# Optimization experiments

Measured on AMD Instinct MI355X. Metric: run time of the kernel, lower is better.

## Reference

```python
import jax, jax.numpy as jnp
import numpy as np

B, S, H = 16, 2048, 1024

def setup_inputs() -> dict:
    key = jax.random.key(0)
    ks = jax.random.split(key, 6)
    return {
        "h": jax.random.normal(ks[0], (1, B, H), jnp.float32),
        "c": jax.random.normal(ks[1], (1, B, H), jnp.float32),
        "encoder_outputs": jax.random.normal(ks[2], (B, S, H), jnp.float32),
        "attn_W": jax.random.normal(ks[3], (H, 2 * H), jnp.float32) * 0.02,
        "attn_b": jax.random.normal(ks[4], (H,), jnp.float32) * 0.02,
        "v_W": jax.random.normal(ks[5], (1, H), jnp.float32) * 0.02,
    }

def reference(h, c, encoder_outputs, attn_W, attn_b, v_W):
    # h: (1,B,H) -> (B,1,H); a: (B,S,H)
    a = encoder_outputs
    hq = jnp.transpose(h, (1, 0, 2))  # (B,1,H)
    # cat((s, a), -1) @ attn_W.T == s @ Wh.T + a @ Wa.T (avoids (B,S,2H) buffer)
    Wh, Wa = attn_W[:, :H], attn_W[:, H:]
    energy = jax.nn.relu(
        jnp.einsum("bqh,oh->bqo", hq, Wh)          # (B,1,H), broadcast over S
        + jnp.einsum("bsh,oh->bso", a, Wa)
        + attn_b
    )  # (B,S,H)
    scores = jnp.einsum("bsh,h->bs", energy, v_W[0])  # (B,S)
    attn_weights = jax.nn.softmax(scores, axis=1)      # (B,S)
    context = jnp.einsum("bs,bsh->bh", attn_weights, a)[:, None, :]  # (B,1,H)
    return context, attn_weights
```

## Files before the change

kernel.cpp:

```cpp
#include <hip/hip_runtime.h>
#include <hip/hip_bf16.h>


typedef __bf16 bf16x8 __attribute__((ext_vector_type(8)));
typedef float floatx4 __attribute__((ext_vector_type(4)));

#define BB 16
#define SS 2048
#define HH 1024
#define MM (BB * SS)

#define GLB(p) ((const __attribute__((address_space(1))) void*)(p))
#define LDSP(p) ((__attribute__((address_space(3))) void*)(p))

__device__ inline ushort f2bf(float x) {
    uint32_t u = __builtin_bit_cast(uint32_t, x);
    u += 0x7FFFu + ((u >> 16) & 1u);
    return (ushort)(u >> 16);
}

__global__ __launch_bounds__(256) void prep_all_kernel(
    const float* __restrict__ h, const float* __restrict__ W,
    const float* __restrict__ bias, const float* __restrict__ a,
    float* __restrict__ projh, __bf16* __restrict__ Wb, __bf16* __restrict__ Ab,
    float* __restrict__ sp0, float* __restrict__ ctx)
{
    int bid = blockIdx.x;
    int tid = threadIdx.x;
    if (bid >= 336) {
        size_t i = (size_t)(bid - 336) * 256 + tid;
        const float* s = a + i * 8;
        float4 x = *(const float4*)(s);
        float4 y = *(const float4*)(s + 4);
        union { ushort u[8]; uint4 v; } p;
        p.u[0] = f2bf(x.x); p.u[1] = f2bf(x.y); p.u[2] = f2bf(x.z); p.u[3] = f2bf(x.w);
        p.u[4] = f2bf(y.x); p.u[5] = f2bf(y.y); p.u[6] = f2bf(y.z); p.u[7] = f2bf(y.w);
        *(uint4*)(Ab + i * 8) = p.v;
    } else if (bid < 256) {
        int b = bid >> 4;
        int oc = bid & 15;
        __shared__ float hrow[HH];
        *(float4*)&hrow[tid * 4] = *(const float4*)(h + (size_t)b * HH + tid * 4);
        __syncthreads();
        int ol = tid >> 2;
        int kq = tid & 3;
        int o = oc * 64 + ol;
        const float* wr = W + (size_t)o * (2 * HH) + kq * 256;
        const float* hb = hrow + kq * 256;
        float sum = 0.f;
        for (int k = 0; k < 256; k += 4) {
            float4 wv = *(const float4*)(wr + k);
            sum += hb[k] * wv.x + hb[k + 1] * wv.y + hb[k + 2] * wv.z + hb[k + 3] * wv.w;
        }
        sum += __shfl_xor(sum, 1);
        sum += __shfl_xor(sum, 2);
        if (kq == 0) projh[b * HH + o] = sum + bias[o];
    } else if (bid < 320) {
        int cb = bid - 256;
#pragma unroll
        for (int j = 0; j < 8; j++) {
            int g = cb * 2048 + tid + j * 256;
            int o = g >> 7;
            int k = (g & 127) * 8;
            const float* s = W + (size_t)o * (2 * HH) + HH + k;
            float4 x = *(const float4*)(s);
            float4 y = *(const float4*)(s + 4);
            union { ushort u[8]; uint4 v; } p;
            p.u[0] = f2bf(x.x); p.u[1] = f2bf(x.y); p.u[2] = f2bf(x.z); p.u[3] = f2bf(x.w);
            p.u[4] = f2bf(y.x); p.u[5] = f2bf(y.y); p.u[6] = f2bf(y.z); p.u[7] = f2bf(y.w);
            *(uint4*)(Wb + (size_t)o * HH + k) = p.v;
        }
    } else {
        int zb = bid - 320;
        float4 z = make_float4(0.f, 0.f, 0.f, 0.f);
        float* sp = sp0 + zb * 2048 + tid * 8;
        *(float4*)(sp) = z;
        *(float4*)(sp + 4) = z;
        *(float4*)(ctx + zb * 1024 + tid * 4) = z;
    }
}

__global__ __launch_bounds__(512, 2) void gemm_scores_kernel(
    const __bf16* __restrict__ Ab,
    const __bf16* __restrict__ Wb,
    const float* __restrict__ projh,
    const float* __restrict__ vW,
    float* __restrict__ scores_part)
{
    __shared__ __bf16 smem[65536];

    const int bid = blockIdx.x;
    const int m0 = (((bid >> 5) << 3) + (bid & 7)) * 256;
    const int nq = (bid >> 3) & 3;
    const int n0 = nq * 256;
    const int bidx = m0 >> 11;

    const int tid = threadIdx.x;
    const int lane = tid & 63;
    const int wave = tid >> 6;
    const int wm = (wave & 1) * 128;
    const int wn = (wave >> 1) * 64;
    const int quad = lane >> 4;
    const int l16 = lane & 15;

    floatx4 acc[8][4];
    const floatx4 z = {0.f, 0.f, 0.f, 0.f};
#pragma unroll
    for (int i = 0; i < 8; i++)
#pragma unroll
        for (int j = 0; j < 4; j++) acc[i][j] = z;

    const int su = tid >> 3;
    const int sj = (tid & 7) ^ (su & 7);
    const int g_row = su * 2 + (sj >> 2);
    const int g_col = (sj & 3) * 8;
    const __bf16* gA0 = Ab + (size_t)(m0 + g_row) * HH + g_col;
    const __bf16* gA1 = gA0 + (size_t)128 * HH;
    const __bf16* gB0 = Wb + (size_t)(n0 + g_row) * HH + g_col;
    const __bf16* gB1 = gB0 + (size_t)128 * HH;
    const int wchunk = wave * 512;

    int aoff[8], boff[4];
#pragma unroll
    for (int i = 0; i < 8; i++) {
        int frow = wm + i * 16 + l16;
        int r7 = frow & 127;
        int u2 = r7 >> 1;
        int cc = u2 * 8 + (((((r7 & 1) << 2) | quad)) ^ (u2 & 7));
        aoff[i] = (frow >> 7) * 4096 + cc * 8;
    }
#pragma unroll
    for (int j = 0; j < 4; j++) {
        int frow = wn + j * 16 + l16;
        int r7 = frow & 127;
        int u2 = r7 >> 1;
        int cc = u2 * 8 + (((((r7 & 1) << 2) | quad)) ^ (u2 & 7));
        boff[j] = 32768 + (frow >> 7) * 4096 + cc * 8;
    }

#define STAGE_A(slot, koff)                                                             \
    {                                                                                   \
        __bf16* d_ = smem + (slot) * 8192 + wchunk;                                     \
        __builtin_amdgcn_global_load_lds(GLB(gA0 + (koff)), LDSP(d_), 16, 0, 0);        \
        __builtin_amdgcn_global_load_lds(GLB(gA1 + (koff)), LDSP(d_ + 4096), 16, 0, 0); \
    }
#define STAGE_B(slot, koff)                                                             \
    {                                                                                   \
        __bf16* d_ = smem + 32768 + (slot) * 8192 + wchunk;                             \
        __builtin_amdgcn_global_load_lds(GLB(gB0 + (koff)), LDSP(d_), 16, 0, 0);        \
        __builtin_amdgcn_global_load_lds(GLB(gB1 + (koff)), LDSP(d_ + 4096), 16, 0, 0); \
    }
#define READ_BFR(base)                                     \
    {                                                      \
        bfr[0] = *(const bf16x8*)((base) + boff[0]);       \
        bfr[1] = *(const bf16x8*)((base) + boff[1]);       \
        bfr[2] = *(const bf16x8*)((base) + boff[2]);       \
        bfr[3] = *(const bf16x8*)((base) + boff[3]);       \
    }
#define READ_ALO(base)                                     \
    {                                                      \
        af[0] = *(const bf16x8*)((base) + aoff[0]);        \
        af[1] = *(const bf16x8*)((base) + aoff[1]);        \
        af[2] = *(const bf16x8*)((base) + aoff[2]);        \
        af[3] = *(const bf16x8*)((base) + aoff[3]);        \
    }
#define READ_AHI(base)                                     \
    {                                                      \
        af2[0] = *(const bf16x8*)((base) + aoff[4]);       \
        af2[1] = *(const bf16x8*)((base) + aoff[5]);       \
        af2[2] = *(const bf16x8*)((base) + aoff[6]);       \
        af2[3] = *(const bf16x8*)((base) + aoff[7]);       \
    }
#define MFMA_LO                                                                            \
    _Pragma("unroll") for (int i_ = 0; i_ < 4; i_++)                                       \
        _Pragma("unroll") for (int j_ = 0; j_ < 4; j_++)                                   \
            acc[i_][j_] = __builtin_amdgcn_mfma_f32_16x16x32_bf16(af[i_], bfr[j_], acc[i_][j_], 0, 0, 0);
#define MFMA_HI                                                                            \
    _Pragma("unroll") for (int i_ = 0; i_ < 4; i_++)                                       \
        _Pragma("unroll") for (int j_ = 0; j_ < 4; j_++)                                   \
            acc[i_ + 4][j_] = __builtin_amdgcn_mfma_f32_16x16x32_bf16(af2[i_], bfr[j_], acc[i_ + 4][j_], 0, 0, 0);
#define BAR __builtin_amdgcn_s_barrier()
#define LGKM0 asm volatile("s_waitcnt lgkmcnt(0)" ::: "memory")
#define VM8 asm volatile("s_waitcnt vmcnt(8)" ::: "memory")
#define PRIO1 __builtin_amdgcn_s_setprio(1)
#define PRIO0 __builtin_amdgcn_s_setprio(0)

#define SPAN(P, K1, K2)                              \
    {                                                \
        const __bf16* cb0 = smem + (P) * 16384;      \
        const __bf16* cb1 = cb0 + 8192;              \
                                        \
        READ_BFR(cb0); READ_ALO(cb0);                \
        STAGE_A((1 - (P)) * 2 + 1, K1);              \
        BAR; LGKM0; PRIO1; MFMA_LO; PRIO0; BAR;      \
                                        \
        READ_AHI(cb0);                               \
        STAGE_B((1 - (P)) * 2 + 1, K1);              \
        VM8;                                         \
        BAR; LGKM0; PRIO1; MFMA_HI; PRIO0; BAR;      \
                                        \
        READ_BFR(cb1); READ_ALO(cb1);                \
        STAGE_A((P) * 2, K2);                        \
        BAR; LGKM0; PRIO1; MFMA_LO; PRIO0; BAR;      \
                                        \
        READ_AHI(cb1);                               \
        STAGE_B((P) * 2, K2);                        \
        VM8;                                         \
        BAR; LGKM0; PRIO1; MFMA_HI; PRIO0; BAR;      \
    }

    bf16x8 af[4], af2[4], bfr[4];

    STAGE_A(0, 0);  STAGE_B(0, 0);
    STAGE_A(1, 32); STAGE_B(1, 32);
    STAGE_A(2, 64); STAGE_B(2, 64);
    VM8;
    BAR;

    for (int it = 0; it < 8; ++it) {
        const int kb = it * 128;
        const int k1 = kb + 96;
        const int k2 = (it < 7) ? kb + 128 : 0;
        const int k3 = (it < 7) ? kb + 160 : 0;
        const int k4 = (it < 7) ? kb + 192 : 0;
        SPAN(0, k1, k2)
        SPAN(1, k3, k4)
    }

#undef SPAN
#undef STAGE_A
#undef STAGE_B
#undef READ_BFR
#undef READ_ALO
#undef READ_AHI
#undef MFMA_LO
#undef MFMA_HI
#undef BAR
#undef LGKM0
#undef VM8
#undef PRIO1
#undef PRIO0

    float ph[4], vv[4];
#pragma unroll
    for (int j = 0; j < 4; j++) {
        int ng = n0 + wn + j * 16 + l16;
        ph[j] = projh[bidx * HH + ng];
        vv[j] = vW[ng];
    }

    float* red = (float*)smem;
    if (tid < 256) red[tid] = 0.f;
    __syncthreads();

#pragma unroll
    for (int i = 0; i < 8; i++) {
        float s[4] = {0.f, 0.f, 0.f, 0.f};
#pragma unroll
        for (int j = 0; j < 4; j++) {
#pragma unroll
            for (int r2 = 0; r2 < 4; r2++) {
                float e = acc[i][j][r2] + ph[j];
                e = e > 0.f ? e : 0.f;
                s[r2] += e * vv[j];
            }
        }
#pragma unroll
        for (int r2 = 0; r2 < 4; r2++) {
            s[r2] += __shfl_xor(s[r2], 1);
            s[r2] += __shfl_xor(s[r2], 2);
            s[r2] += __shfl_xor(s[r2], 4);
            s[r2] += __shfl_xor(s[r2], 8);
        }
        if (l16 == 0) {
#pragma unroll
            for (int r2 = 0; r2 < 4; r2++)
                atomicAdd(&red[wm + i * 16 + quad * 4 + r2], s[r2]);
        }
    }
    __syncthreads();
    if (tid < 256) scores_part[(size_t)nq * MM + m0 + tid] = red[tid];
}

__global__ __launch_bounds__(256) void gemm_scores_f32_kernel(
    const float* __restrict__ A, const float* __restrict__ W,
    const float* __restrict__ projh, const float* __restrict__ vW,
    float* __restrict__ scores)
{
    constexpr int BM = 128, BN = 128, BK = 32, LDT = BK + 8;
    __shared__ __bf16 As[BM * LDT];
    __shared__ __bf16 Bs[BN * LDT];
    const int n0 = blockIdx.x * BN;
    const int m0 = blockIdx.y * BM;
    const int bidx = m0 >> 11;
    const int tid = threadIdx.x;
    const int lane = tid & 63;
    const int wave = tid >> 6;
    const int wm = (wave & 1) * 64;
    const int wn = (wave >> 1) * 64;
    const int quad = lane >> 4;
    const int l16 = lane & 15;
    floatx4 acc[4][4];
    const floatx4 z = {0.f, 0.f, 0.f, 0.f};
#pragma unroll
    for (int i = 0; i < 4; i++)
#pragma unroll
        for (int j = 0; j < 4; j++) acc[i][j] = z;
    int rowT[4], colT[4];
#pragma unroll
    for (int i = 0; i < 4; i++) {
        int fi = tid + 256 * i;
        rowT[i] = fi >> 3;
        colT[i] = (fi & 7) * 4;
    }
    for (int k0 = 0; k0 < HH; k0 += BK) {
        float4 av[4], bv[4];
#pragma unroll
        for (int i = 0; i < 4; i++) {
            av[i] = *(const float4*)(A + (size_t)(m0 + rowT[i]) * HH + k0 + colT[i]);
            bv[i] = *(const float4*)(W + (size_t)(n0 + rowT[i]) * (2 * HH) + HH + k0 + colT[i]);
        }
        __syncthreads();
#pragma unroll
        for (int i = 0; i < 4; i++) {
            ushort4 ua = make_ushort4(f2bf(av[i].x), f2bf(av[i].y), f2bf(av[i].z), f2bf(av[i].w));
            ushort4 ub = make_ushort4(f2bf(bv[i].x), f2bf(bv[i].y), f2bf(bv[i].z), f2bf(bv[i].w));
            *(ushort4*)&As[rowT[i] * LDT + colT[i]] = ua;
            *(ushort4*)&Bs[rowT[i] * LDT + colT[i]] = ub;
        }
        __syncthreads();
        bf16x8 af[4], bf[4];
#pragma unroll
        for (int i = 0; i < 4; i++)
            af[i] = *(const bf16x8*)&As[(wm + i * 16 + l16) * LDT + quad * 8];
#pragma unroll
        for (int j = 0; j < 4; j++)
            bf[j] = *(const bf16x8*)&Bs[(wn + j * 16 + l16) * LDT + quad * 8];
#pragma unroll
        for (int i = 0; i < 4; i++)
#pragma unroll
            for (int j = 0; j < 4; j++)
                acc[i][j] = __builtin_amdgcn_mfma_f32_16x16x32_bf16(af[i], bf[j], acc[i][j], 0, 0, 0);
    }
    float ph[4], vv[4];
#pragma unroll
    for (int j = 0; j < 4; j++) {
        int ng = n0 + wn + j * 16 + l16;
        ph[j] = projh[bidx * HH + ng];
        vv[j] = vW[ng];
    }
#pragma unroll
    for (int i = 0; i < 4; i++) {
        float s[4] = {0.f, 0.f, 0.f, 0.f};
#pragma unroll
        for (int j = 0; j < 4; j++) {
#pragma unroll
            for (int r = 0; r < 4; r++) {
                float e = acc[i][j][r] + ph[j];
                e = e > 0.f ? e : 0.f;
                s[r] += e * vv[j];
            }
        }
#pragma unroll
        for (int r = 0; r < 4; r++) {
            s[r] += __shfl_xor(s[r], 1);
            s[r] += __shfl_xor(s[r], 2);
            s[r] += __shfl_xor(s[r], 4);
            s[r] += __shfl_xor(s[r], 8);
        }
        if (l16 == 0) {
#pragma unroll
            for (int r = 0; r < 4; r++) {
                int mg = m0 + wm + i * 16 + quad * 4 + r;
                atomicAdd(&scores[mg], s[r]);
            }
        }
    }
}

__global__ __launch_bounds__(256) void softmax_context_kernel(
    const __bf16* __restrict__ Ab, const float* __restrict__ scores_part,
    int nparts, float* __restrict__ wout, float* __restrict__ ctx)
{
    int b = blockIdx.x >> 5;
    int sc = blockIdx.x & 31;
    int tid = threadIdx.x;
    const float* srow = scores_part + b * SS;

    float x[8];
    float mx = -1e30f;
#pragma unroll
    for (int i = 0; i < 8; i++) {
        int idx = tid + i * 256;
        float v = srow[idx];
        for (int q = 1; q < nparts; q++) v += srow[(size_t)q * MM + idx];
        x[i] = v; mx = fmaxf(mx, v);
    }
#pragma unroll
    for (int off = 32; off; off >>= 1) mx = fmaxf(mx, __shfl_xor(mx, off));
    __shared__ float redm[4], reds[4];
    if ((tid & 63) == 0) redm[tid >> 6] = mx;
    __syncthreads();
    mx = fmaxf(fmaxf(redm[0], redm[1]), fmaxf(redm[2], redm[3]));
    float sum = 0.f;
#pragma unroll
    for (int i = 0; i < 8; i++) sum += __expf(x[i] - mx);
#pragma unroll
    for (int off = 32; off; off >>= 1) sum += __shfl_xor(sum, off);
    if ((tid & 63) == 0) reds[tid >> 6] = sum;
    __syncthreads();
    float inv = 1.0f / (reds[0] + reds[1] + reds[2] + reds[3]);

    __shared__ float wsm[64];
    if (tid < 64) {
        int idx = sc * 64 + tid;
        float v = srow[idx];
        for (int q = 1; q < nparts; q++) v += srow[(size_t)q * MM + idx];
        float wv = __expf(v - mx) * inv;
        wsm[tid] = wv;
        wout[b * SS + idx] = wv;
    }
    __syncthreads();

    const __bf16* arow = Ab + ((size_t)b * SS + sc * 64) * HH + tid * 4;
    float4 acc = make_float4(0.f, 0.f, 0.f, 0.f);
#pragma unroll 4
    for (int s = 0; s < 64; s++) {
        float w = wsm[s];
        uint2 uv = *(const uint2*)(arow + (size_t)s * HH);
        float a0 = __builtin_bit_cast(float, uv.x << 16);
        float a1 = __builtin_bit_cast(float, uv.x & 0xffff0000u);
        float a2 = __builtin_bit_cast(float, uv.y << 16);
        float a3 = __builtin_bit_cast(float, uv.y & 0xffff0000u);
        acc.x += w * a0; acc.y += w * a1; acc.z += w * a2; acc.w += w * a3;
    }
    float* o = ctx + b * HH + tid * 4;
    atomicAdd(o + 0, acc.x);
    atomicAdd(o + 1, acc.y);
    atomicAdd(o + 2, acc.z);
    atomicAdd(o + 3, acc.w);
}

__global__ __launch_bounds__(256) void softmax_context_f32_kernel(
    const float* __restrict__ A, const float* __restrict__ scores_part,
    float* __restrict__ wout, float* __restrict__ ctx)
{
    int b = blockIdx.x >> 5;
    int sc = blockIdx.x & 31;
    int tid = threadIdx.x;
    const float* srow = scores_part + b * SS;
    float x[8];
    float mx = -1e30f;
#pragma unroll
    for (int i = 0; i < 8; i++) { x[i] = srow[tid + i * 256]; mx = fmaxf(mx, x[i]); }
#pragma unroll
    for (int off = 32; off; off >>= 1) mx = fmaxf(mx, __shfl_xor(mx, off));
    __shared__ float redm[4], reds[4];
    if ((tid & 63) == 0) redm[tid >> 6] = mx;
    __syncthreads();
    mx = fmaxf(fmaxf(redm[0], redm[1]), fmaxf(redm[2], redm[3]));
    float sum = 0.f;
#pragma unroll
    for (int i = 0; i < 8; i++) sum += __expf(x[i] - mx);
#pragma unroll
    for (int off = 32; off; off >>= 1) sum += __shfl_xor(sum, off);
    if ((tid & 63) == 0) reds[tid >> 6] = sum;
    __syncthreads();
    float inv = 1.0f / (reds[0] + reds[1] + reds[2] + reds[3]);
    __shared__ float wsm[64];
    if (tid < 64) {
        float wv = __expf(srow[sc * 64 + tid] - mx) * inv;
        wsm[tid] = wv;
        wout[b * SS + sc * 64 + tid] = wv;
    }
    __syncthreads();
    const float* arow = A + ((size_t)b * SS + sc * 64) * HH + tid * 4;
    float4 acc = make_float4(0.f, 0.f, 0.f, 0.f);
#pragma unroll 4
    for (int s = 0; s < 64; s++) {
        float w = wsm[s];
        float4 v = *(const float4*)(arow + (size_t)s * HH);
        acc.x += w * v.x; acc.y += w * v.y; acc.z += w * v.z; acc.w += w * v.w;
    }
    float* o = ctx + b * HH + tid * 4;
    atomicAdd(o + 0, acc.x);
    atomicAdd(o + 1, acc.y);
    atomicAdd(o + 2, acc.z);
    atomicAdd(o + 3, acc.w);
}

extern "C" void kernel_launch(void* const* d_in, const int* in_sizes, int n_in,
                              void* d_out, int out_size, void* d_ws, size_t ws_size,
                              hipStream_t stream) {
    const float* h    = (const float*)d_in[0];
    const float* a    = (const float*)d_in[2];
    const float* W    = (const float*)d_in[3];
    const float* bias = (const float*)d_in[4];
    const float* vW   = (const float*)d_in[5];
    float* out = (float*)d_out;

    float* projh       = (float*)d_ws;
    float* scores_part = projh + BB * HH;
    __bf16* Wb = (__bf16*)(scores_part + 4 * MM);
    __bf16* Ab = Wb + (size_t)HH * HH;
    const size_t need = (size_t)(BB * HH + 4 * MM) * 4 + (size_t)HH * HH * 2
                      + (size_t)MM * HH * 2;

    if (ws_size >= need) {
        prep_all_kernel<<<336 + MM * HH / 8 / 256, 256, 0, stream>>>(
            h, W, bias, a, projh, Wb, Ab, scores_part, out);
        gemm_scores_kernel<<<512, 512, 0, stream>>>(Ab, Wb, projh, vW, scores_part);
        softmax_context_kernel<<<BB * 32, 256, 0, stream>>>(
            Ab, scores_part, 4, out + BB * HH, out);
    } else {
        prep_all_kernel<<<336, 256, 0, stream>>>(h, W, bias, a, projh, Wb, Ab, scores_part, out);
        gemm_scores_f32_kernel<<<dim3(HH / 128, MM / 128), 256, 0, stream>>>(
            a, W, projh, vW, scores_part);
        softmax_context_f32_kernel<<<BB * 32, 256, 0, stream>>>(
            a, scores_part, out + BB * HH, out);
    }
}
```

Baseline: 292.3 us.

## Fuse fp32-to-bf16 conversion of encoder outputs into GEMM A-tile staging

Removes the separate prep pass that converted the full encoder_outputs tensor to bf16. The GEMM now loads fp32 A tiles into registers, converts them and writes them to LDS. Blocks with nq==0 also write the bf16 copy to global memory for the later softmax/context kernel. This saves one full fp32 read and bf16 write pass over the 128MB input. In exchange, A loads go through registers instead of direct global-to-LDS copies, with new vmcnt waits, and each A tile is read in fp32 by all four N-quarter blocks.

After: 319.2 us. 1.09x slower.

```diff
diff --git a/kernel.cpp b/kernel.cpp
--- a/kernel.cpp
+++ b/kernel.cpp
@@ -21,22 +21,13 @@
 
 __global__ __launch_bounds__(256) void prep_all_kernel(
     const float* __restrict__ h, const float* __restrict__ W,
-    const float* __restrict__ bias, const float* __restrict__ a,
-    float* __restrict__ projh, __bf16* __restrict__ Wb, __bf16* __restrict__ Ab,
+    const float* __restrict__ bias,
+    float* __restrict__ projh, __bf16* __restrict__ Wb,
     float* __restrict__ sp0, float* __restrict__ ctx)
 {
     int bid = blockIdx.x;
     int tid = threadIdx.x;
-    if (bid >= 336) {
-        size_t i = (size_t)(bid - 336) * 256 + tid;
-        const float* s = a + i * 8;
-        float4 x = *(const float4*)(s);
-        float4 y = *(const float4*)(s + 4);
-        union { ushort u[8]; uint4 v; } p;
-        p.u[0] = f2bf(x.x); p.u[1] = f2bf(x.y); p.u[2] = f2bf(x.z); p.u[3] = f2bf(x.w);
-        p.u[4] = f2bf(y.x); p.u[5] = f2bf(y.y); p.u[6] = f2bf(y.z); p.u[7] = f2bf(y.w);
-        *(uint4*)(Ab + i * 8) = p.v;
-    } else if (bid < 256) {
+    if (bid < 256) {
         int b = bid >> 4;
         int oc = bid & 15;
         __shared__ float hrow[HH];
@@ -81,11 +72,12 @@
 }
 
 __global__ __launch_bounds__(512, 2) void gemm_scores_kernel(
-    const __bf16* __restrict__ Ab,
+    const float* __restrict__ Af,
     const __bf16* __restrict__ Wb,
     const float* __restrict__ projh,
     const float* __restrict__ vW,
-    float* __restrict__ scores_part)
+    float* __restrict__ scores_part,
+    __bf16* __restrict__ Ab)
 {
     __shared__ __bf16 smem[65536];
 
@@ -114,8 +106,10 @@
     const int sj = (tid & 7) ^ (su & 7);
     const int g_row = su * 2 + (sj >> 2);
     const int g_col = (sj & 3) * 8;
-    const __bf16* gA0 = Ab + (size_t)(m0 + g_row) * HH + g_col;
-    const __bf16* gA1 = gA0 + (size_t)128 * HH;
+    const float* gAf0 = Af + (size_t)(m0 + g_row) * HH + g_col;
+    const float* gAf1 = gAf0 + (size_t)128 * HH;
+    __bf16* abw0 = Ab + (size_t)(m0 + g_row) * HH + g_col;
+    __bf16* abw1 = abw0 + (size_t)128 * HH;
     const __bf16* gB0 = Wb + (size_t)(n0 + g_row) * HH + g_col;
     const __bf16* gB1 = gB0 + (size_t)128 * HH;
     const int wchunk = wave * 512;
@@ -138,17 +132,36 @@
         boff[j] = 32768 + (frow >> 7) * 4096 + cc * 8;
     }
 
-#define STAGE_A(slot, koff)                                                             \
-    {                                                                                   \
-        __bf16* d_ = smem + (slot) * 8192 + wchunk;                                     \
-        __builtin_amdgcn_global_load_lds(GLB(gA0 + (koff)), LDSP(d_), 16, 0, 0);        \
-        __builtin_amdgcn_global_load_lds(GLB(gA1 + (koff)), LDSP(d_ + 4096), 16, 0, 0); \
-    }
-#define STAGE_B(slot, koff)                                                             \
+#define BGLOAD(slot, koff)                                                              \
     {                                                                                   \
         __bf16* d_ = smem + 32768 + (slot) * 8192 + wchunk;                             \
         __builtin_amdgcn_global_load_lds(GLB(gB0 + (koff)), LDSP(d_), 16, 0, 0);        \
         __builtin_amdgcn_global_load_lds(GLB(gB1 + (koff)), LDSP(d_ + 4096), 16, 0, 0); \
+    }
+#define AISSUE(K)                                      \
+    {                                                  \
+        ar0 = *(const float4*)(gAf0 + (K));            \
+        ar1 = *(const float4*)(gAf0 + (K) + 4);        \
+        ar2 = *(const float4*)(gAf1 + (K));            \
+        ar3 = *(const float4*)(gAf1 + (K) + 4);        \
+    }
+#define AWRITE(x0, x1, x2, x3, slot, K, WBOK)                                           \
+    {                                                                                   \
+        union { ushort u[8]; uint4 v; } pl_, ph_;                                       \
+        pl_.u[0] = f2bf((x0).x); pl_.u[1] = f2bf((x0).y);                               \
+        pl_.u[2] = f2bf((x0).z); pl_.u[3] = f2bf((x0).w);                               \
+        pl_.u[4] = f2bf((x1).x); pl_.u[5] = f2bf((x1).y);                               \
+        pl_.u[6] = f2bf((x1).z); pl_.u[7] = f2bf((x1).w);                               \
+        ph_.u[0] = f2bf((x2).x); ph_.u[1] = f2bf((x2).y);                               \
+        ph_.u[2] = f2bf((x2).z); ph_.u[3] = f2bf((x2).w);                               \
+        ph_.u[4] = f2bf((x3).x); ph_.u[5] = f2bf((x3).y);                               \
+        ph_.u[6] = f2bf((x3).z); ph_.u[7] = f2bf((x3).w);                               \
+        *(uint4*)(smem + (slot) * 8192 + tid * 8) = pl_.v;                              \
+        *(uint4*)(smem + (slot) * 8192 + 4096 + tid * 8) = ph_.v;                       \
+        if ((WBOK) && nq == 0) {                                                        \
+            *(uint4*)(abw0 + (K)) = pl_.v;                                              \
+            *(uint4*)(abw1 + (K)) = ph_.v;                                              \
+        }                                                                               \
     }
 #define READ_BFR(base)                                     \
     {                                                      \
@@ -181,55 +194,80 @@
             acc[i_ + 4][j_] = __builtin_amdgcn_mfma_f32_16x16x32_bf16(af2[i_], bfr[j_], acc[i_ + 4][j_], 0, 0, 0);
 #define BAR __builtin_amdgcn_s_barrier()
 #define LGKM0 asm volatile("s_waitcnt lgkmcnt(0)" ::: "memory")
-#define VM8 asm volatile("s_waitcnt vmcnt(8)" ::: "memory")
+#define VMW2 asm volatile("s_waitcnt vmcnt(2)" ::: "memory")
+#define VMW8 asm volatile("s_waitcnt vmcnt(8)" ::: "memory")
+#define VMW0 asm volatile("s_waitcnt vmcnt(0)" ::: "memory")
 #define PRIO1 __builtin_amdgcn_s_setprio(1)
 #define PRIO0 __builtin_amdgcn_s_setprio(0)
 
-#define SPAN(P, K1, K2)                              \
+#define SPAN(P, K1, K2, K3, WB1, WB2)                \
     {                                                \
         const __bf16* cb0 = smem + (P) * 16384;      \
         const __bf16* cb1 = cb0 + 8192;              \
                                         \
         READ_BFR(cb0); READ_ALO(cb0);                \
-        STAGE_A((1 - (P)) * 2 + 1, K1);              \
+        VMW2;                                        \
+        AWRITE(ar0, ar1, ar2, ar3, (1 - (P)) * 2 + 1, K1, WB1); \
+        AISSUE(K2);                                  \
         BAR; LGKM0; PRIO1; MFMA_LO; PRIO0; BAR;      \
                                         \
         READ_AHI(cb0);                               \
-        STAGE_B((1 - (P)) * 2 + 1, K1);              \
-        VM8;                                         \
+        BGLOAD((1 - (P)) * 2 + 1, K1);               \
         BAR; LGKM0; PRIO1; MFMA_HI; PRIO0; BAR;      \
                                         \
         READ_BFR(cb1); READ_ALO(cb1);                \
-        STAGE_A((P) * 2, K2);                        \
+        VMW2;                                        \
+        AWRITE(ar0, ar1, ar2, ar3, (P) * 2, K2, WB2); \
+        AISSUE(K3);                                  \
         BAR; LGKM0; PRIO1; MFMA_LO; PRIO0; BAR;      \
                                         \
         READ_AHI(cb1);                               \
-        STAGE_B((P) * 2, K2);                        \
-        VM8;                                         \
+        BGLOAD((P) * 2, K2);                         \
         BAR; LGKM0; PRIO1; MFMA_HI; PRIO0; BAR;      \
     }
 
     bf16x8 af[4], af2[4], bfr[4];
-
-    STAGE_A(0, 0);  STAGE_B(0, 0);
-    STAGE_A(1, 32); STAGE_B(1, 32);
-    STAGE_A(2, 64); STAGE_B(2, 64);
-    VM8;
-    BAR;
+    float4 ar0, ar1, ar2, ar3;
+
+    {
+        float4 t0, t1, t2, t3, u0, u1, u2, u3;
+        t0 = *(const float4*)(gAf0 + 0);  t1 = *(const float4*)(gAf0 + 4);
+        t2 = *(const float4*)(gAf1 + 0);  t3 = *(const float4*)(gAf1 + 4);
+        u0 = *(const float4*)(gAf0 + 32); u1 = *(const float4*)(gAf0 + 36);
+        u2 = *(const float4*)(gAf1 + 32); u3 = *(const float4*)(gAf1 + 36);
+        BGLOAD(0, 0);
+        BGLOAD(1, 32);
+        VMW8;
+        AWRITE(t0, t1, t2, t3, 0, 0, true);
+        t0 = *(const float4*)(gAf0 + 64); t1 = *(const float4*)(gAf0 + 68);
+        t2 = *(const float4*)(gAf1 + 64); t3 = *(const float4*)(gAf1 + 68);
+        VMW8;
+        AWRITE(u0, u1, u2, u3, 1, 32, true);
+        VMW0;
+        AWRITE(t0, t1, t2, t3, 2, 64, true);
+        AISSUE(96);
+        BGLOAD(2, 64);
+        LGKM0;
+        BAR;
+    }
 
     for (int it = 0; it < 8; ++it) {
         const int kb = it * 128;
-        const int k1 = kb + 96;
-        const int k2 = (it < 7) ? kb + 128 : 0;
-        const int k3 = (it < 7) ? kb + 160 : 0;
-        const int k4 = (it < 7) ? kb + 192 : 0;
-        SPAN(0, k1, k2)
-        SPAN(1, k3, k4)
+        const bool e = (it < 7);
+        const int K1a = kb + 96;
+        const int K2a = e ? kb + 128 : 0;
+        const int K3a = e ? kb + 160 : 0;
+        const int K1b = e ? kb + 160 : 0;
+        const int K2b = e ? kb + 192 : 0;
+        const int K3b = e ? kb + 224 : 0;
+        SPAN(0, K1a, K2a, K3a, true, e)
+        SPAN(1, K1b, K2b, K3b, e, e)
     }
 
 #undef SPAN
-#undef STAGE_A
-#undef STAGE_B
+#undef BGLOAD
+#undef AISSUE
+#undef AWRITE
 #undef READ_BFR
 #undef READ_ALO
 #undef READ_AHI
@@ -237,7 +275,9 @@
 #undef MFMA_HI
 #undef BAR
 #undef LGKM0
-#undef VM8
+#undef VMW2
+#undef VMW8
+#undef VMW0
 #undef PRIO1
 #undef PRIO0
 
@@ -507,13 +547,12 @@
                       + (size_t)MM * HH * 2;
 
     if (ws_size >= need) {
-        prep_all_kernel<<<336 + MM * HH / 8 / 256, 256, 0, stream>>>(
-            h, W, bias, a, projh, Wb, Ab, scores_part, out);
-        gemm_scores_kernel<<<512, 512, 0, stream>>>(Ab, Wb, projh, vW, scores_part);
+        prep_all_kernel<<<336, 256, 0, stream>>>(h, W, bias, projh, Wb, scores_part, out);
+        gemm_scores_kernel<<<512, 512, 0, stream>>>(a, Wb, projh, vW, scores_part, Ab);
         softmax_context_kernel<<<BB * 32, 256, 0, stream>>>(
             Ab, scores_part, 4, out + BB * HH, out);
     } else {
-        prep_all_kernel<<<336, 256, 0, stream>>>(h, W, bias, a, projh, Wb, Ab, scores_part, out);
+        prep_all_kernel<<<336, 256, 0, stream>>>(h, W, bias, projh, Wb, scores_part, out);
         gemm_scores_f32_kernel<<<dim3(HH / 128, MM / 128), 256, 0, stream>>>(
             a, W, projh, vW, scores_part);
         softmax_context_f32_kernel<<<BB * 32, 256, 0, stream>>>(
```
